# Optimization experiments

Hardware: AMD Instinct MI355X
Metric: run time of the kernel (lower is better)

Reference implementation:

```python
import jax, jax.numpy as jnp
import numpy as np

N = 50000
E = 800000
NEG_SLOPE = 0.2


def setup_inputs() -> dict:
    key = jax.random.key(0)
    ks = jax.random.split(key, 12)
    feat = jax.random.normal(ks[0], (N, 256), dtype=jnp.float32)
    src = jax.random.randint(ks[1], (E,), 0, N, dtype=jnp.int32)
    dst = jax.random.randint(ks[2], (E,), 0, N, dtype=jnp.int32)
    # layer 1: in=256 -> H=4, D=64 (concat 256)
    W1 = jax.random.normal(ks[3], (256, 256), dtype=jnp.float32) * (1.0 / np.sqrt(256))
    attn_l1 = jax.random.normal(ks[4], (4, 64), dtype=jnp.float32) * 0.1
    attn_r1 = jax.random.normal(ks[5], (4, 64), dtype=jnp.float32) * 0.1
    bias1 = jnp.zeros((256,), dtype=jnp.float32)
    # layer 2: in=256 -> H=1, D=128
    W2 = jax.random.normal(ks[6], (256, 128), dtype=jnp.float32) * (1.0 / np.sqrt(256))
    attn_l2 = jax.random.normal(ks[7], (1, 128), dtype=jnp.float32) * 0.1
    attn_r2 = jax.random.normal(ks[8], (1, 128), dtype=jnp.float32) * 0.1
    bias2 = jnp.zeros((128,), dtype=jnp.float32)
    return {"feat": feat, "src": src, "dst": dst,
            "W1": W1, "attn_l1": attn_l1, "attn_r1": attn_r1, "bias1": bias1,
            "W2": W2, "attn_l2": attn_l2, "attn_r2": attn_r2, "bias2": bias2}


def gat_conv(feat, src, dst, W, attn_l, attn_r, bias, apply_relu):
    H, D = attn_l.shape
    n = feat.shape[0]
    ft = (feat @ W).reshape(n, H, D)                      # [N,H,D]
    el = jnp.einsum('nhd,hd->nh', ft, attn_l)             # [N,H]
    er = jnp.einsum('nhd,hd->nh', ft, attn_r)             # [N,H]
    e = el[src] + er[dst]                                 # [E,H]  u_add_v
    e = jnp.where(e > 0, e, NEG_SLOPE * e)                # leaky_relu
    # edge softmax grouped by dst
    m = jax.ops.segment_max(e, dst, num_segments=n)       # [N,H]
    ex = jnp.exp(e - m[dst])
    denom = jax.ops.segment_sum(ex, dst, num_segments=n)  # [N,H]
    a = ex / denom[dst]                                   # [E,H]
    msg = ft[src] * a[:, :, None]                         # [E,H,D]
    out = jax.ops.segment_sum(msg, dst, num_segments=n)   # [N,H,D]
    out = out + bias.reshape(1, H, D)
    out = out.reshape(n, H * D)                           # concat_out
    if apply_relu:
        out = jax.nn.relu(out)
    return out


def reference(feat, src, dst, W1, attn_l1, attn_r1, bias1, W2, attn_l2, attn_r2, bias2):
    h = gat_conv(feat, src, dst, W1, attn_l1, attn_r1, bias1, apply_relu=True)
    h = gat_conv(h, src, dst, W2, attn_l2, attn_r2, bias2, apply_relu=False)
    return h
```

## Files before the change

kernel.cpp:

```cpp
#include <hip/hip_runtime.h>
#include <hip/hip_bf16.h>

#define NEG_SLOPE 0.2f

typedef short s16x8 __attribute__((ext_vector_type(8)));
typedef float f32x4 __attribute__((ext_vector_type(4)));

__device__ __forceinline__ unsigned short f2bf(float f) {
    unsigned int u = __float_as_uint(f);
    unsigned int r = (u + 0x7fffu + ((u >> 16) & 1u)) >> 16;
    return (unsigned short)r;
}
__device__ __forceinline__ float bf2f(unsigned int us) {
    return __uint_as_float(us << 16);
}


__global__ void count_wl_k(const int* __restrict__ dst, int* __restrict__ counts, int E,
                           const float* __restrict__ W1, const float* __restrict__ al1,
                           const float* __restrict__ ar1,
                           const float* __restrict__ W2, const float* __restrict__ al2,
                           const float* __restrict__ ar2,
                           float* __restrict__ wl1, float* __restrict__ wl2) {
    if (blockIdx.x == 0) {
        int k = threadIdx.x;
        #pragma unroll
        for (int h = 0; h < 4; h++) {
            float sl = 0.f, sr = 0.f;
            #pragma unroll 8
            for (int d = 0; d < 64; d++) {
                float wv = W1[k * 256 + h * 64 + d];
                sl = fmaf(wv, al1[h * 64 + d], sl);
                sr = fmaf(wv, ar1[h * 64 + d], sr);
            }
            wl1[k * 8 + h] = sl;
            wl1[k * 8 + 4 + h] = sr;
        }
        float sl = 0.f, sr = 0.f;
        #pragma unroll 8
        for (int d = 0; d < 128; d++) {
            float wv = W2[k * 128 + d];
            sl = fmaf(wv, al2[d], sl);
            sr = fmaf(wv, ar2[d], sr);
        }
        wl2[k * 2 + 0] = sl;
        wl2[k * 2 + 1] = sr;
        return;
    }
    int e = (blockIdx.x - 1) * 256 + threadIdx.x;
    if (e < E) atomicAdd(&counts[dst[e]], 1);
}


__global__ __launch_bounds__(1024) void scan_k(const int* __restrict__ counts,
                                               int* __restrict__ flags,
                                               int* __restrict__ offsets,
                                               int* __restrict__ cursor, int n) {
    __shared__ int s_wt[16];
    __shared__ int s_base;
    const int tid = threadIdx.x, lane = tid & 63, wid = tid >> 6;
    const int bid = blockIdx.x;
    const int i = bid * 1024 + tid;
    int v = (i < n) ? counts[i] : 0;
    int incl = v;
    #pragma unroll
    for (int o = 1; o < 64; o <<= 1) {
        int t = __shfl_up(incl, o);
        if (lane >= o) incl += t;
    }
    if (lane == 63) s_wt[wid] = incl;
    __syncthreads();
    if (tid == 0) {
        int r = 0;
        #pragma unroll
        for (int w = 0; w < 16; w++) { int t = s_wt[w]; s_wt[w] = r; r += t; }
        atomicExch(&flags[bid], r + 1);
        s_base = 0;
    }
    __syncthreads();
    if (wid == 0) {
        int contrib = 0;
        if (lane < bid) {
            int f;
            while ((f = atomicAdd(&flags[lane], 0)) == 0) {}
            contrib = f - 1;
        }
        #pragma unroll
        for (int o = 32; o > 0; o >>= 1) contrib += __shfl_xor(contrib, o);
        if (lane == 0) s_base = contrib;
    }
    __syncthreads();
    if (i < n) {
        int excl = s_base + s_wt[wid] + (incl - v);
        offsets[i + 1] = excl + v;
        cursor[i] = excl;
    }
    if (bid == 0 && tid == 0) offsets[0] = 0;
}

__global__ void fill_csr_k(const int* __restrict__ src, const int* __restrict__ dst,
                           int* __restrict__ cursor, int* __restrict__ csr_src, int E) {
    int e = blockIdx.x * blockDim.x + threadIdx.x;
    if (e < E) {
        int pos = atomicAdd(&cursor[dst[e]], 1);
        csr_src[pos] = src[e];
    }
}


template <int MODE>
__global__ __launch_bounds__(256) void gemm_k(const float* __restrict__ A,
                                              const float* __restrict__ B,
                                              unsigned short* __restrict__ Cb,
                                              int M, int K, int Nc,
                                              const float* __restrict__ wl,
                                              float* __restrict__ el,
                                              float* __restrict__ er) {
    __shared__ __align__(16) unsigned short As_hi[128][40], As_lo[128][40];
    __shared__ __align__(16) unsigned short Bs_hi[64][40],  Bs_lo[64][40];
    __shared__ float s_wla[256], s_wlb[256];
    __shared__ float s_red[128][2];

    const int tid = threadIdx.x;
    const int lane = tid & 63, wid = tid >> 6;
    const int row0 = blockIdx.x * 128;
    const int by = blockIdx.y;
    const int col0 = by * 64;
    const int wm = (wid & 1) * 64;
    const int wn = (wid >> 1) * 32;
    const int quad = lane >> 4, mrow = lane & 15;

    const int a_r = tid >> 1;
    const int a_k = (tid & 1) * 16;
    const int b_k = tid >> 3;
    const int b_n = (tid & 7) * 8;
    const bool a_valid = (row0 + a_r) < M;

    if (MODE == 1) { s_wla[tid] = wl[tid * 8 + by]; s_wlb[tid] = wl[tid * 8 + 4 + by]; }
    else           { s_wla[tid] = wl[tid * 2 + by]; }
    __syncthreads();

    f32x4 acc[4][2];
    #pragma unroll
    for (int i = 0; i < 4; i++)
        #pragma unroll
        for (int j = 0; j < 2; j++) acc[i][j] = f32x4{0.f, 0.f, 0.f, 0.f};
    float pa = 0.f, pb = 0.f;

    for (int k0 = 0; k0 < K; k0 += 32) {
        float af[16];
        if (a_valid) {
            const float* ap = &A[(size_t)(row0 + a_r) * K + k0 + a_k];
            #pragma unroll
            for (int q = 0; q < 4; q++) {
                float4 t = *(const float4*)(ap + q * 4);
                af[q * 4 + 0] = t.x; af[q * 4 + 1] = t.y;
                af[q * 4 + 2] = t.z; af[q * 4 + 3] = t.w;
            }
        } else {
            #pragma unroll
            for (int q = 0; q < 16; q++) af[q] = 0.f;
        }
        #pragma unroll
        for (int p = 0; p < 16; p++) {
            pa = fmaf(af[p], s_wla[k0 + a_k + p], pa);
            if (MODE == 1) pb = fmaf(af[p], s_wlb[k0 + a_k + p], pb);
        }
        unsigned int* dh = (unsigned int*)&As_hi[a_r][a_k];
        unsigned int* dl = (unsigned int*)&As_lo[a_r][a_k];
        #pragma unroll
        for (int p = 0; p < 8; p++) {
            unsigned short h0 = f2bf(af[2 * p]), h1 = f2bf(af[2 * p + 1]);
            unsigned short l0 = f2bf(af[2 * p] - bf2f(h0));
            unsigned short l1 = f2bf(af[2 * p + 1] - bf2f(h1));
            dh[p] = (unsigned int)h0 | ((unsigned int)h1 << 16);
            dl[p] = (unsigned int)l0 | ((unsigned int)l1 << 16);
        }
        {
            const float* bp = &B[(size_t)(k0 + b_k) * Nc + col0 + b_n];
            float4 t0 = *(const float4*)(bp);
            float4 t1 = *(const float4*)(bp + 4);
            float bf[8] = {t0.x, t0.y, t0.z, t0.w, t1.x, t1.y, t1.z, t1.w};
            #pragma unroll
            for (int x = 0; x < 8; x++) {
                unsigned short h = f2bf(bf[x]);
                unsigned short l = f2bf(bf[x] - bf2f(h));
                Bs_hi[b_n + x][b_k] = h;
                Bs_lo[b_n + x][b_k] = l;
            }
        }
        __syncthreads();

        s16x8 ah[4], al4[4], bh[2], bl[2];
        #pragma unroll
        for (int i = 0; i < 4; i++) {
            ah[i]  = *(const s16x8*)&As_hi[wm + 16 * i + mrow][quad * 8];
            al4[i] = *(const s16x8*)&As_lo[wm + 16 * i + mrow][quad * 8];
        }
        #pragma unroll
        for (int j = 0; j < 2; j++) {
            bh[j] = *(const s16x8*)&Bs_hi[wn + 16 * j + mrow][quad * 8];
            bl[j] = *(const s16x8*)&Bs_lo[wn + 16 * j + mrow][quad * 8];
        }
        #pragma unroll
        for (int i = 0; i < 4; i++)
            #pragma unroll
            for (int j = 0; j < 2; j++) {
                acc[i][j] = __builtin_amdgcn_mfma_f32_16x16x32_bf16(ah[i],  bh[j], acc[i][j], 0, 0, 0);
                acc[i][j] = __builtin_amdgcn_mfma_f32_16x16x32_bf16(ah[i],  bl[j], acc[i][j], 0, 0, 0);
                acc[i][j] = __builtin_amdgcn_mfma_f32_16x16x32_bf16(al4[i], bh[j], acc[i][j], 0, 0, 0);
            }
        __syncthreads();
    }

    if (a_k == 16) { s_red[a_r][0] = pa; if (MODE == 1) s_red[a_r][1] = pb; }
    __syncthreads();
    if (a_k == 0 && a_valid) {
        float ra = pa + s_red[a_r][0];
        if (MODE == 1) {
            float rb = pb + s_red[a_r][1];
            el[(row0 + a_r) * 4 + by] = ra;
            er[(row0 + a_r) * 4 + by] = rb;
        } else {
            (by == 0 ? el : er)[row0 + a_r] = ra;
        }
    }

    #pragma unroll
    for (int i = 0; i < 4; i++) {
        #pragma unroll
        for (int j = 0; j < 2; j++) {
            int col = col0 + wn + 16 * j + mrow;
            int rbase = row0 + wm + 16 * i + quad * 4;
            #pragma unroll
            for (int r = 0; r < 4; r++) {
                int row = rbase + r;
                if (row < M) Cb[(size_t)row * Nc + col] = f2bf(acc[i][j][r]);
            }
        }
    }
}


template <int H>
__device__ __forceinline__ void edge_e(const float* __restrict__ el, int sv,
                                       const float* ern, float* e) {
    if constexpr (H == 4) {
        float4 e4 = ((const float4*)el)[sv];
        float tmp[4] = {e4.x, e4.y, e4.z, e4.w};
        #pragma unroll
        for (int h = 0; h < 4; h++) {
            float t = tmp[h] + ern[h];
            e[h] = t > 0.f ? t : NEG_SLOPE * t;
        }
    } else {
        float t = el[sv] + ern[0];
        e[0] = t > 0.f ? t : NEG_SLOPE * t;
    }
}

template <int H, int CPL>
__device__ __forceinline__ void gather_edges(const unsigned short* __restrict__ ft,
                                             const int* s_src_w, const float* s_a_w,
                                             int i0, int cnt, int lane, int h_of,
                                             float* acc) {
    int i = i0;
    if constexpr (CPL == 4) {
        const uint2* fp = ((const uint2*)ft) + lane;
        for (; i + 8 <= cnt; i += 8) {
            int ss[8]; float ww[8]; uint2 uu[8];
            #pragma unroll
            for (int u = 0; u < 8; u++) ss[u] = s_src_w[i + u];
            #pragma unroll
            for (int u = 0; u < 8; u++) uu[u] = fp[(size_t)ss[u] * 64];
            #pragma unroll
            for (int u = 0; u < 8; u++) ww[u] = s_a_w[(i + u) * H + h_of];
            #pragma unroll
            for (int u = 0; u < 8; u++) {
                acc[0] = fmaf(ww[u], bf2f(uu[u].x & 0xffff), acc[0]);
                acc[1] = fmaf(ww[u], bf2f(uu[u].x >> 16), acc[1]);
                acc[2] = fmaf(ww[u], bf2f(uu[u].y & 0xffff), acc[2]);
                acc[3] = fmaf(ww[u], bf2f(uu[u].y >> 16), acc[3]);
            }
        }
        for (; i < cnt; i++) {
            float w = s_a_w[i * H + h_of];
            uint2 u = fp[(size_t)s_src_w[i] * 64];
            acc[0] = fmaf(w, bf2f(u.x & 0xffff), acc[0]);
            acc[1] = fmaf(w, bf2f(u.x >> 16), acc[1]);
            acc[2] = fmaf(w, bf2f(u.y & 0xffff), acc[2]);
            acc[3] = fmaf(w, bf2f(u.y >> 16), acc[3]);
        }
    } else {
        const unsigned int* fp = ((const unsigned int*)ft) + lane;
        for (; i + 8 <= cnt; i += 8) {
            int ss[8]; float ww[8]; unsigned int uu[8];
            #pragma unroll
            for (int u = 0; u < 8; u++) ss[u] = s_src_w[i + u];
            #pragma unroll
            for (int u = 0; u < 8; u++) uu[u] = fp[(size_t)ss[u] * 64];
            #pragma unroll
            for (int u = 0; u < 8; u++) ww[u] = s_a_w[(i + u) * H + h_of];
            #pragma unroll
            for (int u = 0; u < 8; u++) {
                acc[0] = fmaf(ww[u], bf2f(uu[u] & 0xffff), acc[0]);
                acc[1] = fmaf(ww[u], bf2f(uu[u] >> 16), acc[1]);
            }
        }
        for (; i < cnt; i++) {
            float w = s_a_w[i * H + h_of];
            unsigned int u = fp[(size_t)s_src_w[i] * 64];
            acc[0] = fmaf(w, bf2f(u & 0xffff), acc[0]);
            acc[1] = fmaf(w, bf2f(u >> 16), acc[1]);
        }
    }
}

template <int H, int D, bool RELU>
__global__ __launch_bounds__(256) void fagg_k(const unsigned short* __restrict__ ft,
                                              const float* __restrict__ el,
                                              const float* __restrict__ er,
                                              const int* __restrict__ offsets,
                                              const int* __restrict__ csr_src,
                                              const float* __restrict__ bias,
                                              float* __restrict__ out, int n_nodes) {
    constexpr int HD = H * D;
    constexpr int CPL = HD / 64;
    const int lane = threadIdx.x & 63;
    const int w = threadIdx.x >> 6;
    const int n = blockIdx.x * 4 + w;
    __shared__ int   s_src[4][64];
    __shared__ float s_a[4][64 * H];
    if (n >= n_nodes) return;
    const int off = offsets[n];
    const int deg = offsets[n + 1] - off;
    const int c0 = lane * CPL;
    const int h_of = c0 / D;

    float ern[H];
    #pragma unroll
    for (int h = 0; h < H; h++) ern[h] = er[n * H + h];

    float acc[CPL];
    #pragma unroll
    for (int t = 0; t < CPL; t++) acc[t] = 0.f;

    const int* s_src_w = s_src[w];
    const float* s_a_w = s_a[w];

    if (deg > 0 && deg <= 64) {
        const bool act = lane < deg;
        int sv = 0;
        if (act) { sv = csr_src[off + lane]; s_src[w][lane] = sv; }
        float4 elv = float4{0.f, 0.f, 0.f, 0.f};
        float el1v = 0.f;
        if constexpr (H == 4) { if (act) elv = ((const float4*)el)[sv]; }
        else                  { if (act) el1v = el[sv]; }
        const int P = deg < 8 ? deg : 8;
        uint2 pre4[8]; unsigned int pre2[8];
        if constexpr (CPL == 4) {
            const uint2* fp = ((const uint2*)ft) + lane;
            #pragma unroll
            for (int u = 0; u < 8; u++)
                if (u < P) { int su = __shfl(sv, u); pre4[u] = fp[(size_t)su * 64]; }
        } else {
            const unsigned int* fp = ((const unsigned int*)ft) + lane;
            #pragma unroll
            for (int u = 0; u < 8; u++)
                if (u < P) { int su = __shfl(sv, u); pre2[u] = fp[(size_t)su * 64]; }
        }
        float ev[H];
        if constexpr (H == 4) {
            float tmp[4] = {elv.x, elv.y, elv.z, elv.w};
            #pragma unroll
            for (int h = 0; h < 4; h++) {
                float t = tmp[h] + ern[h];
                t = t > 0.f ? t : NEG_SLOPE * t;
                ev[h] = act ? t : -1e30f;
            }
        } else {
            float t = el1v + ern[0];
            t = t > 0.f ? t : NEG_SLOPE * t;
            ev[0] = act ? t : -1e30f;
        }
        float m[H];
        #pragma unroll
        for (int h = 0; h < H; h++) m[h] = ev[h];
        #pragma unroll
        for (int h = 0; h < H; h++)
            for (int o = 32; o > 0; o >>= 1) m[h] = fmaxf(m[h], __shfl_xor(m[h], o));
        float ex[H], sm[H];
        #pragma unroll
        for (int h = 0; h < H; h++) { ex[h] = act ? __expf(ev[h] - m[h]) : 0.f; sm[h] = ex[h]; }
        #pragma unroll
        for (int h = 0; h < H; h++)
            for (int o = 32; o > 0; o >>= 1) sm[h] += __shfl_xor(sm[h], o);
        if (act) {
            #pragma unroll
            for (int h = 0; h < H; h++)
                s_a[w][lane * H + h] = ex[h] * (sm[h] > 0.f ? 1.f / sm[h] : 0.f);
        }
        if constexpr (CPL == 4) {
            #pragma unroll
            for (int u = 0; u < 8; u++)
                if (u < P) {
                    float wgt = s_a_w[u * H + h_of];
                    acc[0] = fmaf(wgt, bf2f(pre4[u].x & 0xffff), acc[0]);
                    acc[1] = fmaf(wgt, bf2f(pre4[u].x >> 16), acc[1]);
                    acc[2] = fmaf(wgt, bf2f(pre4[u].y & 0xffff), acc[2]);
                    acc[3] = fmaf(wgt, bf2f(pre4[u].y >> 16), acc[3]);
                }
        } else {
            #pragma unroll
            for (int u = 0; u < 8; u++)
                if (u < P) {
                    float wgt = s_a_w[u * H + h_of];
                    acc[0] = fmaf(wgt, bf2f(pre2[u] & 0xffff), acc[0]);
                    acc[1] = fmaf(wgt, bf2f(pre2[u] >> 16), acc[1]);
                }
        }
        gather_edges<H, CPL>(ft, s_src_w, s_a_w, P, deg, lane, h_of, acc);
    } else if (deg > 64) {
        float m[H];
        #pragma unroll
        for (int h = 0; h < H; h++) m[h] = -1e30f;
        for (int i = lane; i < deg; i += 64) {
            float e[H];
            edge_e<H>(el, csr_src[off + i], ern, e);
            #pragma unroll
            for (int h = 0; h < H; h++) m[h] = fmaxf(m[h], e[h]);
        }
        #pragma unroll
        for (int h = 0; h < H; h++)
            for (int o = 32; o > 0; o >>= 1) m[h] = fmaxf(m[h], __shfl_xor(m[h], o));
        float sm[H];
        #pragma unroll
        for (int h = 0; h < H; h++) sm[h] = 0.f;
        for (int i = lane; i < deg; i += 64) {
            float e[H];
            edge_e<H>(el, csr_src[off + i], ern, e);
            #pragma unroll
            for (int h = 0; h < H; h++) sm[h] += __expf(e[h] - m[h]);
        }
        #pragma unroll
        for (int h = 0; h < H; h++)
            for (int o = 32; o > 0; o >>= 1) sm[h] += __shfl_xor(sm[h], o);
        float inv[H];
        #pragma unroll
        for (int h = 0; h < H; h++) inv[h] = (sm[h] > 0.f) ? (1.f / sm[h]) : 0.f;
        for (int base = 0; base < deg; base += 64) {
            int cnt = min(64, deg - base);
            if (lane < cnt) {
                int sv = csr_src[off + base + lane];
                float e[H];
                edge_e<H>(el, sv, ern, e);
                s_src[w][lane] = sv;
                #pragma unroll
                for (int h = 0; h < H; h++)
                    s_a[w][lane * H + h] = __expf(e[h] - m[h]) * inv[h];
            }
            gather_edges<H, CPL>(ft, s_src_w, s_a_w, 0, cnt, lane, h_of, acc);
        }
    }

    if constexpr (CPL == 4) {
        float4 b4 = ((const float4*)bias)[lane];
        float v0 = acc[0] + b4.x, v1 = acc[1] + b4.y, v2 = acc[2] + b4.z, v3 = acc[3] + b4.w;
        if (RELU) { v0 = fmaxf(v0, 0.f); v1 = fmaxf(v1, 0.f); v2 = fmaxf(v2, 0.f); v3 = fmaxf(v3, 0.f); }
        ((float4*)out)[(size_t)n * 64 + lane] = float4{v0, v1, v2, v3};
    } else {
        float2 b2 = ((const float2*)bias)[lane];
        float v0 = acc[0] + b2.x, v1 = acc[1] + b2.y;
        if (RELU) { v0 = fmaxf(v0, 0.f); v1 = fmaxf(v1, 0.f); }
        ((float2*)out)[(size_t)n * 64 + lane] = float2{v0, v1};
    }
}


extern "C" void kernel_launch(void* const* d_in, const int* in_sizes, int n_in,
                              void* d_out, int out_size, void* d_ws, size_t ws_size,
                              hipStream_t stream) {
    const float* feat    = (const float*)d_in[0];
    const int*   src     = (const int*)d_in[1];
    const int*   dst     = (const int*)d_in[2];
    const float* W1      = (const float*)d_in[3];
    const float* attn_l1 = (const float*)d_in[4];
    const float* attn_r1 = (const float*)d_in[5];
    const float* bias1   = (const float*)d_in[6];
    const float* W2      = (const float*)d_in[7];
    const float* attn_l2 = (const float*)d_in[8];
    const float* attn_r2 = (const float*)d_in[9];
    const float* bias2   = (const float*)d_in[10];
    float* out = (float*)d_out;

    const int N = in_sizes[0] / 256;
    const int E = in_sizes[1];
    const int NB = (N + 1023) / 1024;

    char* ws = (char*)d_ws;
    size_t o = 0;
    auto alloc = [&](size_t bytes) -> void* {
        void* p = ws + o;
        o = (o + bytes + 255) & ~(size_t)255;
        return p;
    };
    int* counts  = (int*)alloc((size_t)(N + 64) * 4);
    int* flags   = counts + N;
    int* cursor  = (int*)alloc((size_t)N * 4);
    int* offsets = (int*)alloc((size_t)(N + 1) * 4);
    int* csr_src = (int*)alloc((size_t)E * 4);
    float* wl1 = (float*)alloc(256 * 8 * 4);
    float* wl2 = (float*)alloc(256 * 2 * 4);
    float* el1 = (float*)alloc((size_t)N * 4 * 4);
    float* er1 = (float*)alloc((size_t)N * 4 * 4);
    float* el2 = (float*)alloc((size_t)N * 4);
    float* er2 = (float*)alloc((size_t)N * 4);
    unsigned short* ft1b = (unsigned short*)alloc((size_t)N * 256 * 2);
    float* h1 = (float*)alloc((size_t)N * 256 * 4);
    unsigned short* ft2b = ft1b;

    hipMemsetAsync(counts, 0, (size_t)(N + 64) * 4, stream);
    count_wl_k<<<1 + (E + 255) / 256, 256, 0, stream>>>(dst, counts, E,
        W1, attn_l1, attn_r1, W2, attn_l2, attn_r2, wl1, wl2);
    scan_k<<<NB, 1024, 0, stream>>>(counts, flags, offsets, cursor, N);
    fill_csr_k<<<(E + 255) / 256, 256, 0, stream>>>(src, dst, cursor, csr_src, E);

    gemm_k<1><<<dim3((N + 127) / 128, 4), 256, 0, stream>>>(feat, W1, ft1b, N, 256, 256,
                                                            wl1, el1, er1);
    fagg_k<4, 64, true><<<(N + 3) / 4, 256, 0, stream>>>(ft1b, el1, er1, offsets, csr_src,
                                                         bias1, h1, N);

    gemm_k<2><<<dim3((N + 127) / 128, 2), 256, 0, stream>>>(h1, W2, ft2b, N, 256, 128,
                                                            wl2, el2, er2);
    fagg_k<1, 128, false><<<(N + 3) / 4, 256, 0, stream>>>(ft2b, el2, er2, offsets, csr_src,
                                                           bias2, out, N);
}
```

Measured before the change: 401.2 us.

## Split wavefront lanes across edges with 16-byte gathers and reorder GEMM grid

The aggregation kernel now has each lane load 8 bf16 features (uint4) and splits the wavefront into groups that process different edges at the same time: 2 groups for the 256-wide layer and 4 for the 128-wide layer. Partial sums are combined with a cross-group shuffle reduction before the write. The aim is wider memory transactions and more independent gathers in flight per wave, especially in the narrower second layer. The small-degree path now also handles degree 0 and pads inactive edges with zero weight, at the cost of an extra reduction. The GEMM grid swaps its axes so that column tiles sharing a row block run next to each other, which should improve cache reuse of A.

```diff
diff --git a/kernel.cpp b/kernel.cpp
--- a/kernel.cpp
+++ b/kernel.cpp
@@ -123,8 +123,8 @@
 
     const int tid = threadIdx.x;
     const int lane = tid & 63, wid = tid >> 6;
-    const int row0 = blockIdx.x * 128;
-    const int by = blockIdx.y;
+    const int by = blockIdx.x;
+    const int row0 = blockIdx.y * 128;
     const int col0 = by * 64;
     const int wm = (wid & 1) * 64;
     const int wn = (wid >> 1) * 32;
@@ -242,78 +242,15 @@
 }
 
 
-template <int H>
-__device__ __forceinline__ void edge_e(const float* __restrict__ el, int sv,
-                                       const float* ern, float* e) {
-    if constexpr (H == 4) {
-        float4 e4 = ((const float4*)el)[sv];
-        float tmp[4] = {e4.x, e4.y, e4.z, e4.w};
-        #pragma unroll
-        for (int h = 0; h < 4; h++) {
-            float t = tmp[h] + ern[h];
-            e[h] = t > 0.f ? t : NEG_SLOPE * t;
-        }
-    } else {
-        float t = el[sv] + ern[0];
-        e[0] = t > 0.f ? t : NEG_SLOPE * t;
-    }
-}
-
-template <int H, int CPL>
-__device__ __forceinline__ void gather_edges(const unsigned short* __restrict__ ft,
-                                             const int* s_src_w, const float* s_a_w,
-                                             int i0, int cnt, int lane, int h_of,
-                                             float* acc) {
-    int i = i0;
-    if constexpr (CPL == 4) {
-        const uint2* fp = ((const uint2*)ft) + lane;
-        for (; i + 8 <= cnt; i += 8) {
-            int ss[8]; float ww[8]; uint2 uu[8];
-            #pragma unroll
-            for (int u = 0; u < 8; u++) ss[u] = s_src_w[i + u];
-            #pragma unroll
-            for (int u = 0; u < 8; u++) uu[u] = fp[(size_t)ss[u] * 64];
-            #pragma unroll
-            for (int u = 0; u < 8; u++) ww[u] = s_a_w[(i + u) * H + h_of];
-            #pragma unroll
-            for (int u = 0; u < 8; u++) {
-                acc[0] = fmaf(ww[u], bf2f(uu[u].x & 0xffff), acc[0]);
-                acc[1] = fmaf(ww[u], bf2f(uu[u].x >> 16), acc[1]);
-                acc[2] = fmaf(ww[u], bf2f(uu[u].y & 0xffff), acc[2]);
-                acc[3] = fmaf(ww[u], bf2f(uu[u].y >> 16), acc[3]);
-            }
-        }
-        for (; i < cnt; i++) {
-            float w = s_a_w[i * H + h_of];
-            uint2 u = fp[(size_t)s_src_w[i] * 64];
-            acc[0] = fmaf(w, bf2f(u.x & 0xffff), acc[0]);
-            acc[1] = fmaf(w, bf2f(u.x >> 16), acc[1]);
-            acc[2] = fmaf(w, bf2f(u.y & 0xffff), acc[2]);
-            acc[3] = fmaf(w, bf2f(u.y >> 16), acc[3]);
-        }
-    } else {
-        const unsigned int* fp = ((const unsigned int*)ft) + lane;
-        for (; i + 8 <= cnt; i += 8) {
-            int ss[8]; float ww[8]; unsigned int uu[8];
-            #pragma unroll
-            for (int u = 0; u < 8; u++) ss[u] = s_src_w[i + u];
-            #pragma unroll
-            for (int u = 0; u < 8; u++) uu[u] = fp[(size_t)ss[u] * 64];
-            #pragma unroll
-            for (int u = 0; u < 8; u++) ww[u] = s_a_w[(i + u) * H + h_of];
-            #pragma unroll
-            for (int u = 0; u < 8; u++) {
-                acc[0] = fmaf(ww[u], bf2f(uu[u] & 0xffff), acc[0]);
-                acc[1] = fmaf(ww[u], bf2f(uu[u] >> 16), acc[1]);
-            }
-        }
-        for (; i < cnt; i++) {
-            float w = s_a_w[i * H + h_of];
-            unsigned int u = fp[(size_t)s_src_w[i] * 64];
-            acc[0] = fmaf(w, bf2f(u & 0xffff), acc[0]);
-            acc[1] = fmaf(w, bf2f(u >> 16), acc[1]);
-        }
-    }
+__device__ __forceinline__ void fma8(float* acc, float wgt, uint4 u) {
+    acc[0] = fmaf(wgt, bf2f(u.x & 0xffff), acc[0]);
+    acc[1] = fmaf(wgt, bf2f(u.x >> 16),    acc[1]);
+    acc[2] = fmaf(wgt, bf2f(u.y & 0xffff), acc[2]);
+    acc[3] = fmaf(wgt, bf2f(u.y >> 16),    acc[3]);
+    acc[4] = fmaf(wgt, bf2f(u.z & 0xffff), acc[4]);
+    acc[5] = fmaf(wgt, bf2f(u.z >> 16),    acc[5]);
+    acc[6] = fmaf(wgt, bf2f(u.w & 0xffff), acc[6]);
+    acc[7] = fmaf(wgt, bf2f(u.w >> 16),    acc[7]);
 }
 
 template <int H, int D, bool RELU>
@@ -325,7 +262,8 @@
                                               const float* __restrict__ bias,
                                               float* __restrict__ out, int n_nodes) {
     constexpr int HD = H * D;
-    constexpr int CPL = HD / 64;
+    constexpr int LPE = HD / 8;
+    constexpr int EPI = 64 / LPE;
     const int lane = threadIdx.x & 63;
     const int w = threadIdx.x >> 6;
     const int n = blockIdx.x * 4 + w;
@@ -334,58 +272,51 @@
     if (n >= n_nodes) return;
     const int off = offsets[n];
     const int deg = offsets[n + 1] - off;
-    const int c0 = lane * CPL;
+    const int lane_sub = lane & (LPE - 1);
+    const int q = lane / LPE;
+    const int c0 = lane_sub * 8;
     const int h_of = c0 / D;
 
     float ern[H];
     #pragma unroll
     for (int h = 0; h < H; h++) ern[h] = er[n * H + h];
 
-    float acc[CPL];
+    float acc[8];
     #pragma unroll
-    for (int t = 0; t < CPL; t++) acc[t] = 0.f;
+    for (int t = 0; t < 8; t++) acc[t] = 0.f;
 
     const int* s_src_w = s_src[w];
     const float* s_a_w = s_a[w];
-
-    if (deg > 0 && deg <= 64) {
+    const uint4* fp = ((const uint4*)ft) + lane_sub;
+
+    if (deg <= 64) {
         const bool act = lane < deg;
-        int sv = 0;
-        if (act) { sv = csr_src[off + lane]; s_src[w][lane] = sv; }
-        float4 elv = float4{0.f, 0.f, 0.f, 0.f};
-        float el1v = 0.f;
-        if constexpr (H == 4) { if (act) elv = ((const float4*)el)[sv]; }
-        else                  { if (act) el1v = el[sv]; }
-        const int P = deg < 8 ? deg : 8;
-        uint2 pre4[8]; unsigned int pre2[8];
-        if constexpr (CPL == 4) {
-            const uint2* fp = ((const uint2*)ft) + lane;
-            #pragma unroll
-            for (int u = 0; u < 8; u++)
-                if (u < P) { int su = __shfl(sv, u); pre4[u] = fp[(size_t)su * 64]; }
+        int sv = act ? csr_src[off + lane] : 0;
+        s_src[w][lane] = sv;
+        float evr[H];
+        if constexpr (H == 4) {
+            float4 e4 = ((const float4*)el)[sv];
+            evr[0] = e4.x; evr[1] = e4.y; evr[2] = e4.z; evr[3] = e4.w;
         } else {
-            const unsigned int* fp = ((const unsigned int*)ft) + lane;
-            #pragma unroll
-            for (int u = 0; u < 8; u++)
-                if (u < P) { int su = __shfl(sv, u); pre2[u] = fp[(size_t)su * 64]; }
-        }
-        float ev[H];
-        if constexpr (H == 4) {
-            float tmp[4] = {elv.x, elv.y, elv.z, elv.w};
-            #pragma unroll
-            for (int h = 0; h < 4; h++) {
-                float t = tmp[h] + ern[h];
-                t = t > 0.f ? t : NEG_SLOPE * t;
-                ev[h] = act ? t : -1e30f;
-            }
-        } else {
-            float t = el1v + ern[0];
+            evr[0] = el[sv];
+        }
+        int p0, p1, p2, p3;
+        {
+            p0 = s_src_w[q]; p1 = s_src_w[EPI + q];
+            p2 = s_src_w[2 * EPI + q]; p3 = s_src_w[3 * EPI + q];
+        }
+        uint4 u0 = fp[(size_t)p0 * LPE];
+        uint4 u1 = fp[(size_t)p1 * LPE];
+        uint4 u2 = fp[(size_t)p2 * LPE];
+        uint4 u3 = fp[(size_t)p3 * LPE];
+        float ev[H], m[H];
+        #pragma unroll
+        for (int h = 0; h < H; h++) {
+            float t = evr[h] + ern[h];
             t = t > 0.f ? t : NEG_SLOPE * t;
-            ev[0] = act ? t : -1e30f;
-        }
-        float m[H];
-        #pragma unroll
-        for (int h = 0; h < H; h++) m[h] = ev[h];
+            ev[h] = act ? t : -1e30f;
+            m[h] = ev[h];
+        }
         #pragma unroll
         for (int h = 0; h < H; h++)
             for (int o = 32; o > 0; o >>= 1) m[h] = fmaxf(m[h], __shfl_xor(m[h], o));
@@ -395,40 +326,52 @@
         #pragma unroll
         for (int h = 0; h < H; h++)
             for (int o = 32; o > 0; o >>= 1) sm[h] += __shfl_xor(sm[h], o);
-        if (act) {
-            #pragma unroll
-            for (int h = 0; h < H; h++)
-                s_a[w][lane * H + h] = ex[h] * (sm[h] > 0.f ? 1.f / sm[h] : 0.f);
-        }
-        if constexpr (CPL == 4) {
-            #pragma unroll
-            for (int u = 0; u < 8; u++)
-                if (u < P) {
-                    float wgt = s_a_w[u * H + h_of];
-                    acc[0] = fmaf(wgt, bf2f(pre4[u].x & 0xffff), acc[0]);
-                    acc[1] = fmaf(wgt, bf2f(pre4[u].x >> 16), acc[1]);
-                    acc[2] = fmaf(wgt, bf2f(pre4[u].y & 0xffff), acc[2]);
-                    acc[3] = fmaf(wgt, bf2f(pre4[u].y >> 16), acc[3]);
-                }
-        } else {
-            #pragma unroll
-            for (int u = 0; u < 8; u++)
-                if (u < P) {
-                    float wgt = s_a_w[u * H + h_of];
-                    acc[0] = fmaf(wgt, bf2f(pre2[u] & 0xffff), acc[0]);
-                    acc[1] = fmaf(wgt, bf2f(pre2[u] >> 16), acc[1]);
-                }
-        }
-        gather_edges<H, CPL>(ft, s_src_w, s_a_w, P, deg, lane, h_of, acc);
-    } else if (deg > 64) {
+        #pragma unroll
+        for (int h = 0; h < H; h++)
+            s_a[w][lane * H + h] = ex[h] * (sm[h] > 0.f ? 1.f / sm[h] : 0.f);
+        fma8(acc, s_a_w[(q) * H + h_of], u0);
+        fma8(acc, s_a_w[(EPI + q) * H + h_of], u1);
+        fma8(acc, s_a_w[(2 * EPI + q) * H + h_of], u2);
+        fma8(acc, s_a_w[(3 * EPI + q) * H + h_of], u3);
+        const int rc = (deg + EPI - 1) & ~(EPI - 1);
+        int i = 4 * EPI;
+        for (; i + 4 * EPI <= rc; i += 4 * EPI) {
+            int e0 = i + q, e1 = i + EPI + q, e2 = i + 2 * EPI + q, e3 = i + 3 * EPI + q;
+            int s0 = s_src_w[e0], s1 = s_src_w[e1], s2 = s_src_w[e2], s3 = s_src_w[e3];
+            uint4 v0 = fp[(size_t)s0 * LPE];
+            uint4 v1 = fp[(size_t)s1 * LPE];
+            uint4 v2 = fp[(size_t)s2 * LPE];
+            uint4 v3 = fp[(size_t)s3 * LPE];
+            float w0 = s_a_w[e0 * H + h_of], w1 = s_a_w[e1 * H + h_of];
+            float w2 = s_a_w[e2 * H + h_of], w3 = s_a_w[e3 * H + h_of];
+            fma8(acc, w0, v0); fma8(acc, w1, v1); fma8(acc, w2, v2); fma8(acc, w3, v3);
+        }
+        for (; i < rc; i += EPI) {
+            int e = i + q;
+            int s = s_src_w[e];
+            uint4 v = fp[(size_t)s * LPE];
+            fma8(acc, s_a_w[e * H + h_of], v);
+        }
+    } else {
         float m[H];
         #pragma unroll
         for (int h = 0; h < H; h++) m[h] = -1e30f;
         for (int i = lane; i < deg; i += 64) {
-            float e[H];
-            edge_e<H>(el, csr_src[off + i], ern, e);
-            #pragma unroll
-            for (int h = 0; h < H; h++) m[h] = fmaxf(m[h], e[h]);
+            int sv = csr_src[off + i];
+            if constexpr (H == 4) {
+                float4 e4 = ((const float4*)el)[sv];
+                float tmp[4] = {e4.x, e4.y, e4.z, e4.w};
+                #pragma unroll
+                for (int h = 0; h < 4; h++) {
+                    float t = tmp[h] + ern[h];
+                    t = t > 0.f ? t : NEG_SLOPE * t;
+                    m[h] = fmaxf(m[h], t);
+                }
+            } else {
+                float t = el[sv] + ern[0];
+                t = t > 0.f ? t : NEG_SLOPE * t;
+                m[0] = fmaxf(m[0], t);
+            }
         }
         #pragma unroll
         for (int h = 0; h < H; h++)
@@ -437,10 +380,21 @@
         #pragma unroll
         for (int h = 0; h < H; h++) sm[h] = 0.f;
         for (int i = lane; i < deg; i += 64) {
-            float e[H];
-            edge_e<H>(el, csr_src[off + i], ern, e);
-            #pragma unroll
-            for (int h = 0; h < H; h++) sm[h] += __expf(e[h] - m[h]);
+            int sv = csr_src[off + i];
+            if constexpr (H == 4) {
+                float4 e4 = ((const float4*)el)[sv];
+                float tmp[4] = {e4.x, e4.y, e4.z, e4.w};
+                #pragma unroll
+                for (int h = 0; h < 4; h++) {
+                    float t = tmp[h] + ern[h];
+                    t = t > 0.f ? t : NEG_SLOPE * t;
+                    sm[h] += __expf(t - m[h]);
+                }
+            } else {
+                float t = el[sv] + ern[0];
+                t = t > 0.f ? t : NEG_SLOPE * t;
+                sm[0] += __expf(t - m[0]);
+            }
         }
         #pragma unroll
         for (int h = 0; h < H; h++)
@@ -449,30 +403,68 @@
         #pragma unroll
         for (int h = 0; h < H; h++) inv[h] = (sm[h] > 0.f) ? (1.f / sm[h]) : 0.f;
         for (int base = 0; base < deg; base += 64) {
+            const bool act2 = base + lane < deg;
+            int sv = act2 ? csr_src[off + base + lane] : 0;
+            s_src[w][lane] = sv;
+            float exh[H];
+            if constexpr (H == 4) {
+                float4 e4 = ((const float4*)el)[sv];
+                float tmp[4] = {e4.x, e4.y, e4.z, e4.w};
+                #pragma unroll
+                for (int h = 0; h < 4; h++) {
+                    float t = tmp[h] + ern[h];
+                    t = t > 0.f ? t : NEG_SLOPE * t;
+                    exh[h] = act2 ? __expf(t - m[h]) * inv[h] : 0.f;
+                }
+            } else {
+                float t = el[sv] + ern[0];
+                t = t > 0.f ? t : NEG_SLOPE * t;
+                exh[0] = act2 ? __expf(t - m[0]) * inv[0] : 0.f;
+            }
+            #pragma unroll
+            for (int h = 0; h < H; h++) s_a[w][lane * H + h] = exh[h];
             int cnt = min(64, deg - base);
-            if (lane < cnt) {
-                int sv = csr_src[off + base + lane];
-                float e[H];
-                edge_e<H>(el, sv, ern, e);
-                s_src[w][lane] = sv;
-                #pragma unroll
-                for (int h = 0; h < H; h++)
-                    s_a[w][lane * H + h] = __expf(e[h] - m[h]) * inv[h];
-            }
-            gather_edges<H, CPL>(ft, s_src_w, s_a_w, 0, cnt, lane, h_of, acc);
-        }
-    }
-
-    if constexpr (CPL == 4) {
-        float4 b4 = ((const float4*)bias)[lane];
-        float v0 = acc[0] + b4.x, v1 = acc[1] + b4.y, v2 = acc[2] + b4.z, v3 = acc[3] + b4.w;
-        if (RELU) { v0 = fmaxf(v0, 0.f); v1 = fmaxf(v1, 0.f); v2 = fmaxf(v2, 0.f); v3 = fmaxf(v3, 0.f); }
-        ((float4*)out)[(size_t)n * 64 + lane] = float4{v0, v1, v2, v3};
-    } else {
-        float2 b2 = ((const float2*)bias)[lane];
-        float v0 = acc[0] + b2.x, v1 = acc[1] + b2.y;
-        if (RELU) { v0 = fmaxf(v0, 0.f); v1 = fmaxf(v1, 0.f); }
-        ((float2*)out)[(size_t)n * 64 + lane] = float2{v0, v1};
+            int rc = (cnt + EPI - 1) & ~(EPI - 1);
+            int i = 0;
+            for (; i + 4 * EPI <= rc; i += 4 * EPI) {
+                int e0 = i + q, e1 = i + EPI + q, e2 = i + 2 * EPI + q, e3 = i + 3 * EPI + q;
+                int s0 = s_src_w[e0], s1 = s_src_w[e1], s2 = s_src_w[e2], s3 = s_src_w[e3];
+                uint4 v0 = fp[(size_t)s0 * LPE];
+                uint4 v1 = fp[(size_t)s1 * LPE];
+                uint4 v2 = fp[(size_t)s2 * LPE];
+                uint4 v3 = fp[(size_t)s3 * LPE];
+                float w0 = s_a_w[e0 * H + h_of], w1 = s_a_w[e1 * H + h_of];
+                float w2 = s_a_w[e2 * H + h_of], w3 = s_a_w[e3 * H + h_of];
+                fma8(acc, w0, v0); fma8(acc, w1, v1); fma8(acc, w2, v2); fma8(acc, w3, v3);
+            }
+            for (; i < rc; i += EPI) {
+                int e = i + q;
+                int s = s_src_w[e];
+                uint4 v = fp[(size_t)s * LPE];
+                fma8(acc, s_a_w[e * H + h_of], v);
+            }
+        }
+    }
+
+    #pragma unroll
+    for (int t = 0; t < 8; t++) {
+        #pragma unroll
+        for (int s = LPE; s < 64; s <<= 1) acc[t] += __shfl_xor(acc[t], s);
+    }
+    if (lane < LPE) {
+        float4 b0 = ((const float4*)bias)[lane * 2];
+        float4 b1 = ((const float4*)bias)[lane * 2 + 1];
+        float4 o0{acc[0] + b0.x, acc[1] + b0.y, acc[2] + b0.z, acc[3] + b0.w};
+        float4 o1{acc[4] + b1.x, acc[5] + b1.y, acc[6] + b1.z, acc[7] + b1.w};
+        if (RELU) {
+            o0.x = fmaxf(o0.x, 0.f); o0.y = fmaxf(o0.y, 0.f);
+            o0.z = fmaxf(o0.z, 0.f); o0.w = fmaxf(o0.w, 0.f);
+            o1.x = fmaxf(o1.x, 0.f); o1.y = fmaxf(o1.y, 0.f);
+            o1.z = fmaxf(o1.z, 0.f); o1.w = fmaxf(o1.w, 0.f);
+        }
+        float4* op = (float4*)out + (size_t)n * (HD / 4) + lane * 2;
+        op[0] = o0;
+        op[1] = o1;
     }
 }
 
@@ -525,12 +517,12 @@
     scan_k<<<NB, 1024, 0, stream>>>(counts, flags, offsets, cursor, N);
     fill_csr_k<<<(E + 255) / 256, 256, 0, stream>>>(src, dst, cursor, csr_src, E);
 
-    gemm_k<1><<<dim3((N + 127) / 128, 4), 256, 0, stream>>>(feat, W1, ft1b, N, 256, 256,
+    gemm_k<1><<<dim3(4, (N + 127) / 128), 256, 0, stream>>>(feat, W1, ft1b, N, 256, 256,
                                                             wl1, el1, er1);
     fagg_k<4, 64, true><<<(N + 3) / 4, 256, 0, stream>>>(ft1b, el1, er1, offsets, csr_src,
                                                          bias1, h1, N);
 
-    gemm_k<2><<<dim3((N + 127) / 128, 2), 256, 0, stream>>>(h1, W2, ft2b, N, 256, 128,
+    gemm_k<2><<<dim3(2, (N + 127) / 128), 256, 0, stream>>>(h1, W2, ft2b, N, 256, 128,
                                                             wl2, el2, er2);
     fagg_k<1, 128, false><<<(N + 3) / 4, 256, 0, stream>>>(ft2b, el2, er2, offsets, csr_src,
                                                            bias2, out, N);
```

After: 388.1 us. 1.03x faster.
